# Optimization experiments

Hardware: AMD Instinct MI355X
Metric: run time of the kernel (lower is better)

Reference implementation:

```python
import jax, jax.numpy as jnp
import numpy as np

B, N, H, D, F_IN = 2, 2048, 8, 64, 512  # D = per-head dim (= out_features), H*D = model dim
EPS = 1e-5


def setup_inputs() -> dict:
    key = jax.random.key(0)
    k1, k2, k3 = jax.random.split(key, 3)
    x = jax.random.normal(k1, (B, N, F_IN), dtype=jnp.float32)
    adj = jax.random.randint(k2, (B, N, N), 0, 2, dtype=jnp.int32)
    W_w = jax.random.normal(k3, (F_IN, H * D), dtype=jnp.float32) / np.sqrt(F_IN).astype(np.float32)
    W_b = jnp.zeros((H * D,), dtype=jnp.float32)
    gamma = jnp.ones((H * D,), dtype=jnp.float32)
    beta = jnp.zeros((H * D,), dtype=jnp.float32)
    return {"x": x, "adj": adj, "W_w": W_w, "W_b": W_b, "gamma": gamma, "beta": beta}


def reference(x, adj, W_w, W_b, gamma, beta):
    b, n, _ = x.shape
    # shared projection: q = k = v
    h = (x @ W_w + W_b).reshape(b, n, H, D).transpose(0, 2, 1, 3)  # [B,H,N,D]
    attn = jnp.einsum("bhnd,bhmd->bhnm", h, h) * (D ** -0.5)       # [B,H,N,N]
    mask = (adj[:, None, :, :] != 0)                                 # broadcast over heads
    attn = jnp.where(mask, attn, -jnp.inf)
    attn = jax.nn.softmax(attn, axis=-1)
    out = jnp.einsum("bhnm,bhmd->bhnd", attn, h)                    # [B,H,N,D]
    out = out.transpose(0, 2, 1, 3).reshape(b, n, H * D)
    # LayerNorm over model dim
    mu = out.mean(axis=-1, keepdims=True)
    var = out.var(axis=-1, keepdims=True)
    out = (out - mu) * jax.lax.rsqrt(var + EPS) * gamma + beta
    return out, attn.mean(axis=1)
```

## Files before the change

### kernel.cpp

```cpp
#include <hip/hip_runtime.h>

typedef __attribute__((ext_vector_type(8))) short bf16x8;
typedef __attribute__((ext_vector_type(4))) short bf16x4;
typedef __attribute__((ext_vector_type(4))) float f32x4;
typedef __attribute__((ext_vector_type(2))) float f32x2;
typedef __attribute__((ext_vector_type(4))) _Float16 f16x4;
typedef __attribute__((ext_vector_type(2))) _Float16 f16x2;

static __device__ __forceinline__ f32x4 MFMA_QK(bf16x8 a, bf16x8 b, f32x4 c) {
  return __builtin_amdgcn_mfma_f32_16x16x32_bf16(a, b, c, 0, 0, 0);
}

#if __has_builtin(__builtin_amdgcn_mfma_f32_16x16x16bf16_1k)
static __device__ __forceinline__ f32x4 MFMA_PV(bf16x4 a, bf16x4 b, f32x4 c) {
  return __builtin_amdgcn_mfma_f32_16x16x16bf16_1k(a, b, c, 0, 0, 0);
}
#define PV_EPILOGUE_GUARD()
#else
static __device__ __forceinline__ f32x4 MFMA_PV(bf16x4 a, bf16x4 b, f32x4 c) {
  asm("v_mfma_f32_16x16x16_bf16 %0, %1, %2, %0" : "+v"(c) : "v"(a), "v"(b));
  return c;
}
#define PV_EPILOGUE_GUARD() asm volatile("s_nop 7\ns_nop 7" :::)
#endif

#if __has_builtin(__builtin_amdgcn_exp2f)
#define EXP2(x) __builtin_amdgcn_exp2f(x)
#else
#define EXP2(x) exp2f(x)
#endif

#define NB   2
#define NSEQ 2048
#define NH   8
#define ND   64
#define FIN  512
#define MD   512
#define NTOK (NB * NSEQ)
#define SCALE_LOG2E 0.18033688011112042f

#define XB_ELEMS   (NTOK * FIN)
#define WT_ELEMS   (MD * FIN)
#define HH_ELEMS   (NB * NH * NSEQ * ND)
#define MB_ELEMS   (NTOK * 32)
#define L_ELEMS    (NB * NH * NSEQ)
#define O_ELEMS    (NTOK * MD)
#define NSPLIT_S   8
#define NSPLIT_A   4

static __device__ __forceinline__ unsigned short f2b(float f) {
  union { float f; unsigned u; } c; c.f = f;
  unsigned u = c.u;
  u += 0x7fffu + ((u >> 16) & 1u);
  return (unsigned short)(u >> 16);
}

static __device__ __forceinline__ unsigned pack2(float a, float b) {
#if __has_builtin(__builtin_amdgcn_cvt_pk_bf16_f32)
  auto v = __builtin_amdgcn_cvt_pk_bf16_f32(a, b);
  unsigned r; __builtin_memcpy(&r, &v, 4); return r;
#else
  return (unsigned)f2b(a) | ((unsigned)f2b(b) << 16);
#endif
}

static __device__ __forceinline__ void split8(bf16x8 v, bf16x4* a, bf16x4* b) {
  union { bf16x8 w; bf16x4 h[2]; } u; u.w = v; *a = u.h[0]; *b = u.h[1];
}

__global__ __launch_bounds__(256)
void cvt_kernel(const float* __restrict__ x, const float* __restrict__ W,
                unsigned short* __restrict__ xb, unsigned short* __restrict__ wt) {
  const int t = threadIdx.x;
  if (blockIdx.x < 2048) {
    size_t i = ((size_t)blockIdx.x * 256 + t) * 4;
    f32x4 v = *(const f32x4*)(x + i);
    ushort4 o = make_ushort4(f2b(v[0]), f2b(v[1]), f2b(v[2]), f2b(v[3]));
    *(ushort4*)(xb + i) = o;
  } else {
    int j = ((int)(blockIdx.x - 2048) * 256 + t) * 4;
    int k = j >> 9, n = j & 511;
    f32x4 v = *(const f32x4*)(W + (size_t)k * MD + n);
    wt[(size_t)(n + 0) * FIN + k] = f2b(v[0]);
    wt[(size_t)(n + 1) * FIN + k] = f2b(v[1]);
    wt[(size_t)(n + 2) * FIN + k] = f2b(v[2]);
    wt[(size_t)(n + 3) * FIN + k] = f2b(v[3]);
  }
}

__global__ __launch_bounds__(1024)
void maskpack_kernel(const int* __restrict__ adj, unsigned long long* __restrict__ mb) {
  const int t = threadIdx.x;
  const int gw = blockIdx.x * 16 + (t >> 6);
  const int row = gw >> 5, w64 = gw & 31;
  int a = adj[(size_t)row * NSEQ + w64 * 64 + (t & 63)];
  unsigned long long m = __ballot(a != 0);
  if ((t & 63) == 0) mb[gw] = m;
}

__global__ __launch_bounds__(256, 2)
void proj_kernel(const unsigned short* __restrict__ xb, const unsigned short* __restrict__ wt,
                 const float* __restrict__ bias,
                 unsigned short* __restrict__ h_c, unsigned short* __restrict__ h_v) {
  __shared__ __align__(16) unsigned short sA[64][72];
  __shared__ __align__(16) unsigned short sB[64][72];
  const int t = threadIdx.x;
  const int w = t >> 6, L = t & 63, l15 = L & 15, qd = L >> 4;
  const int bm = blockIdx.x, bn = blockIdx.y;
  const int r = t >> 3, c8 = (t & 7) * 8;
  const f32x4 ZERO4 = {0.f, 0.f, 0.f, 0.f};

  f32x4 acc[4];
  #pragma unroll
  for (int q = 0; q < 4; ++q) acc[q] = ZERO4;

  for (int ks = 0; ks < FIN; ks += 64) {
    __syncthreads();
    *(bf16x8*)&sA[r][c8]      = *(const bf16x8*)&xb[(size_t)(bm*64 + r)      * FIN + ks + c8];
    *(bf16x8*)&sA[r + 32][c8] = *(const bf16x8*)&xb[(size_t)(bm*64 + r + 32) * FIN + ks + c8];
    *(bf16x8*)&sB[r][c8]      = *(const bf16x8*)&wt[(size_t)(bn*64 + r)      * FIN + ks + c8];
    *(bf16x8*)&sB[r + 32][c8] = *(const bf16x8*)&wt[(size_t)(bn*64 + r + 32) * FIN + ks + c8];
    __syncthreads();
    #pragma unroll
    for (int kk = 0; kk < 2; ++kk) {
      bf16x8 af = *(const bf16x8*)&sA[16*w + l15][kk*32 + qd*8];
      #pragma unroll
      for (int q = 0; q < 4; ++q) {
        bf16x8 bf = *(const bf16x8*)&sB[16*q + l15][kk*32 + qd*8];
        acc[q] = MFMA_QK(af, bf, acc[q]);
      }
    }
  }

  #pragma unroll
  for (int q = 0; q < 4; ++q) {
    int feat = bn * 64 + 16 * q + l15;
    int hh = feat >> 6, d = feat & 63;
    float bv = bias[feat];
    int token0 = bm * 64 + 16 * w + qd * 4;
    int b0 = token0 >> 11, nn0 = token0 & 2047;
    size_t hcb = (size_t)(b0 * NH + hh) * HH_ELEMS / (NB * NH);
    unsigned short pk[4];
    #pragma unroll
    for (int rr = 0; rr < 4; ++rr) {
      float v = acc[q][rr] + bv;
      unsigned short bb = f2b(v);
      int n = nn0 + rr;
      size_t idx = hcb + ((size_t)(n >> 4)) * 1024 + (d >> 5) * 512
                 + ((d >> 3) & 3) * 128 + (n & 15) * 8 + (d & 7);
      h_c[idx] = bb;
      pk[rr] = bb;
    }
    size_t vidx = hcb + ((size_t)(nn0 >> 4)) * 1024 + ((d >> 5)) * 512
                + (((nn0 >> 2) & 3) * 16 + (d & 15)) * 8 + ((d >> 4) & 1) * 4;
    *(ushort4*)&h_v[vidx] = make_ushort4(pk[0], pk[1], pk[2], pk[3]);
  }
}

__global__ __launch_bounds__(512, 4)
void stats_kernel(const unsigned short* __restrict__ h_c,
                  const unsigned long long* __restrict__ mb,
                  float* __restrict__ l_part) {
  const int t = threadIdx.x;
  const int h = t >> 6, L = t & 63, l15 = L & 15, qd = L >> 4;
  const int u = blockIdx.x & 7;
  const int b = u >> 2;
  const int rblk = ((int)blockIdx.x >> 3) * 4 + (u & 3);
  const int q8 = blockIdx.y;
  const int n0 = rblk * 32;
  const int qd4 = qd * 4;
  const int lane8 = L * 8;
  const f32x4 ZERO4 = {0.f, 0.f, 0.f, 0.f};

  const unsigned short* hc = h_c + (size_t)(b * NH + h) * (NSEQ * ND);
  bf16x8 qf[2][2];
  #pragma unroll
  for (int g = 0; g < 2; ++g)
    #pragma unroll
    for (int kk = 0; kk < 2; ++kk)
      qf[g][kk] = *(const bf16x8*)&hc[((n0 >> 4) + g) * 1024 + kk * 512 + lane8];

  float lacc[2] = {0.f, 0.f};
  const unsigned long long* mrow = mb + (((size_t)(b * NSEQ + n0 + l15)) << 5) + q8 * 4;

  for (int it = 0; it < 4; ++it) {
    const int c0 = q8 * 256 + it * 64;
    unsigned mlo[2], mhi[2];
    #pragma unroll
    for (int g = 0; g < 2; ++g) {
      unsigned long long m = mrow[g * 512 + it];
      mlo[g] = (unsigned)m; mhi[g] = (unsigned)(m >> 32);
    }
    #pragma unroll
    for (int cc = 0; cc < 4; ++cc) {
      const int cb = (c0 >> 4) + cc;
      bf16x8 kf0 = *(const bf16x8*)&hc[cb * 1024 + lane8];
      bf16x8 kf1 = *(const bf16x8*)&hc[cb * 1024 + 512 + lane8];
      #pragma unroll
      for (int g = 0; g < 2; ++g) {
        f32x4 s = MFMA_QK(kf0, qf[g][0], ZERO4);
        s = MFMA_QK(kf1, qf[g][1], s);
        unsigned nib = (((cc & 2) ? mhi[g] : mlo[g]) >> (((cc & 1) << 4) + qd4)) & 0xFu;
        #pragma unroll
        for (int rr = 0; rr < 4; ++rr) {
          float e = EXP2(s[rr] * SCALE_LOG2E);
          lacc[g] += (nib & (1u << rr)) ? e : 0.f;
        }
      }
    }
  }
  #pragma unroll
  for (int g = 0; g < 2; ++g) {
    float v = lacc[g];
    v += __shfl_xor(v, 16);
    v += __shfl_xor(v, 32);
    if (L < 16)
      l_part[(size_t)q8 * L_ELEMS + (size_t)(b * NH + h) * NSEQ + n0 + g*16 + L] = v;
  }
}

__global__ __launch_bounds__(512, 4)
void attn_kernel(const unsigned short* __restrict__ h_c, const unsigned short* __restrict__ h_v,
                 const unsigned long long* __restrict__ mb, const float* __restrict__ l_part,
                 _Float16* __restrict__ o_part, float* __restrict__ mean_out) {
  const int t = threadIdx.x;
  const int h = t >> 6, L = t & 63, l15 = L & 15, qd = L >> 4;
  const int u = blockIdx.x & 7;
  const int b = u >> 2;
  const int rblk = ((int)blockIdx.x >> 3) * 4 + (u & 3);
  const int quarter = blockIdx.y;
  const int n0 = rblk * 32;
  const int qd4 = qd * 4;
  const int lane8 = L * 8;
  __shared__ __align__(16) unsigned short s_part[2][8][32][72];
  const f32x4 ZERO4 = {0.f, 0.f, 0.f, 0.f};

  const unsigned short* hc = h_c + (size_t)(b * NH + h) * (NSEQ * ND);
  const unsigned short* hv = h_v + (size_t)(b * NH + h) * (NSEQ * ND);

  bf16x8 qf[2][2];
  #pragma unroll
  for (int g = 0; g < 2; ++g)
    #pragma unroll
    for (int kk = 0; kk < 2; ++kk)
      qf[g][kk] = *(const bf16x8*)&hc[((n0 >> 4) + g) * 1024 + kk * 512 + lane8];

  float linv[2];
  #pragma unroll
  for (int g = 0; g < 2; ++g) {
    size_t idx = (size_t)(b * NH + h) * NSEQ + n0 + g*16 + l15;
    float ls = 0.f;
    #pragma unroll
    for (int q = 0; q < NSPLIT_S; ++q) ls += l_part[(size_t)q * L_ELEMS + idx];
    linv[g] = -__log2f(ls);
  }

  f32x4 oacc[2][4];
  #pragma unroll
  for (int g = 0; g < 2; ++g)
    #pragma unroll
    for (int dc = 0; dc < 4; ++dc) oacc[g][dc] = ZERO4;

  const int cr = t >> 4, cc4 = (t & 15) * 4;
  const unsigned long long* mrow = mb + (((size_t)(b * NSEQ + n0 + l15)) << 5) + quarter * 8;

  for (int it = 0; it < 8; ++it) {
    const int c0 = quarter * 512 + it * 64;
    const int buf = it & 1;
    unsigned mlo[2], mhi[2];
    #pragma unroll
    for (int g = 0; g < 2; ++g) {
      unsigned long long m = mrow[g * 512 + it];
      mlo[g] = (unsigned)m; mhi[g] = (unsigned)(m >> 32);
    }
    #pragma unroll
    for (int cc = 0; cc < 4; ++cc) {
      const int cb = (c0 >> 4) + cc;
      bf16x8 kf0 = *(const bf16x8*)&hc[cb * 1024 + lane8];
      bf16x8 kf1 = *(const bf16x8*)&hc[cb * 1024 + 512 + lane8];
      bf16x8 vv0 = *(const bf16x8*)&hv[cb * 1024 + lane8];
      bf16x8 vv1 = *(const bf16x8*)&hv[cb * 1024 + 512 + lane8];
      bf16x4 va[4];
      split8(vv0, &va[0], &va[1]);
      split8(vv1, &va[2], &va[3]);
      #pragma unroll
      for (int g = 0; g < 2; ++g) {
        f32x4 s = MFMA_QK(kf0, qf[g][0], ZERO4);
        s = MFMA_QK(kf1, qf[g][1], s);
        unsigned nib = (((cc & 2) ? mhi[g] : mlo[g]) >> (((cc & 1) << 4) + qd4)) & 0xFu;
        f32x4 p;
        #pragma unroll
        for (int rr = 0; rr < 4; ++rr) {
          float e = EXP2(__builtin_fmaf(s[rr], SCALE_LOG2E, linv[g]));
          p[rr] = (nib & (1u << rr)) ? e : 0.f;
        }
        union { unsigned u2[2]; bf16x4 v4; uint2 d; } pk;
        pk.u2[0] = pack2(p[0], p[1]);
        pk.u2[1] = pack2(p[2], p[3]);
        *(uint2*)&s_part[buf][h][g*16 + l15][cc*16 + qd4] = pk.d;
        #pragma unroll
        for (int dc = 0; dc < 4; ++dc)
          oacc[g][dc] = MFMA_PV(va[dc], pk.v4, oacc[g][dc]);
      }
    }
    __syncthreads();
    {
      f32x4 macc = ZERO4;
      #pragma unroll
      for (int hh = 0; hh < 8; ++hh) {
        uint2 pv = *(const uint2*)&s_part[buf][hh][cr][cc4];
        union { unsigned u; float f; } a0, a1, a2, a3;
        a0.u = pv.x << 16; a1.u = pv.x & 0xffff0000u;
        a2.u = pv.y << 16; a3.u = pv.y & 0xffff0000u;
        macc[0] += a0.f; macc[1] += a1.f; macc[2] += a2.f; macc[3] += a3.f;
      }
      macc *= 0.125f;
      *(f32x4*)&mean_out[((size_t)b * NSEQ + n0 + cr) * NSEQ + c0 + cc4] = macc;
    }
  }

  PV_EPILOGUE_GUARD();
  #pragma unroll
  for (int g = 0; g < 2; ++g)
    #pragma unroll
    for (int dc = 0; dc < 4; ++dc) {
      size_t token = (size_t)b * NSEQ + n0 + g*16 + l15;
      f16x4 o;
      #pragma unroll
      for (int rr = 0; rr < 4; ++rr) o[rr] = (_Float16)oacc[g][dc][rr];
      *(f16x4*)&o_part[(size_t)quarter * O_ELEMS + token * MD + h*64 + dc*16 + qd4] = o;
    }
}

__global__ __launch_bounds__(256)
void ln_kernel(const _Float16* __restrict__ o_part, const float* __restrict__ gamma,
               const float* __restrict__ beta, float* __restrict__ out) {
  const int row = blockIdx.x, t = threadIdx.x;
  const size_t base = (size_t)row * MD + 2 * t;
  float v0 = 0.f, v1 = 0.f;
  #pragma unroll
  for (int q = 0; q < NSPLIT_A; ++q) {
    f16x2 x = *(const f16x2*)&o_part[(size_t)q * O_ELEMS + base];
    v0 += (float)x[0]; v1 += (float)x[1];
  }
  float s = v0 + v1, sq = v0 * v0 + v1 * v1;
  for (int m = 1; m < 64; m <<= 1) { s += __shfl_xor(s, m); sq += __shfl_xor(sq, m); }
  __shared__ float rs[4], rq[4];
  if ((t & 63) == 0) { rs[t >> 6] = s; rq[t >> 6] = sq; }
  __syncthreads();
  s = rs[0] + rs[1] + rs[2] + rs[3];
  sq = rq[0] + rq[1] + rq[2] + rq[3];
  float mu = s * (1.f / MD);
  float var = sq * (1.f / MD) - mu * mu;
  float rstd = rsqrtf(var + 1e-5f);
  f32x2 g2 = *(const f32x2*)&gamma[2 * t];
  f32x2 b2 = *(const f32x2*)&beta[2 * t];
  f32x2 o;
  o[0] = (v0 - mu) * rstd * g2[0] + b2[0];
  o[1] = (v1 - mu) * rstd * g2[1] + b2[1];
  *(f32x2*)&out[base] = o;
}

extern "C" void kernel_launch(void* const* d_in, const int* in_sizes, int n_in,
                              void* d_out, int out_size, void* d_ws, size_t ws_size,
                              hipStream_t stream) {
  const float* x     = (const float*)d_in[0];
  const int*   adj   = (const int*)d_in[1];
  const float* W     = (const float*)d_in[2];
  const float* Wb    = (const float*)d_in[3];
  const float* gamma = (const float*)d_in[4];
  const float* beta  = (const float*)d_in[5];
  float* out = (float*)d_out;

  unsigned short* xb  = (unsigned short*)d_ws;
  unsigned short* wt  = xb + XB_ELEMS;
  unsigned short* h_c = wt + WT_ELEMS;
  unsigned short* h_v = h_c + HH_ELEMS;
  unsigned long long* mbits = (unsigned long long*)(h_v + HH_ELEMS);
  float* l_part = (float*)(mbits + MB_ELEMS);
  _Float16* o_part = (_Float16*)(l_part + NSPLIT_S * L_ELEMS);

  cvt_kernel<<<2304, 256, 0, stream>>>(x, W, xb, wt);
  maskpack_kernel<<<8192, 1024, 0, stream>>>(adj, mbits);
  proj_kernel<<<dim3(64, 8), 256, 0, stream>>>(xb, wt, Wb, h_c, h_v);
  stats_kernel<<<dim3(128, NSPLIT_S), 512, 0, stream>>>(h_c, mbits, l_part);
  attn_kernel<<<dim3(128, NSPLIT_A), 512, 0, stream>>>(h_c, h_v, mbits, l_part, o_part,
                                                       out + (size_t)NTOK * MD);
  ln_kernel<<<NTOK, 256, 0, stream>>>(o_part, gamma, beta, out);
}
```

Baseline: 186.0 us.

## Split attention across eighths with atomic fp32 output and transposed projection stores

The attention kernel's key-column split goes from four to eight, so twice as many blocks launch. Partial outputs are now summed with fp32 atomicAdd into one zeroed buffer, replacing per-quarter fp16 partials that layer norm had to add up. The LDS double buffer for the per-head probabilities becomes a single buffer with an extra barrier. The projection kernel computes a second, transposed MFMA accumulator so h_c can be written with vectorized ushort4 stores instead of scalar scattered stores. The costs are doubled projection MFMA work, a memset, and atomic contention on the output.

```diff
diff --git a/kernel.cpp b/kernel.cpp
--- a/kernel.cpp
+++ b/kernel.cpp
@@ -4,8 +4,6 @@
 typedef __attribute__((ext_vector_type(4))) short bf16x4;
 typedef __attribute__((ext_vector_type(4))) float f32x4;
 typedef __attribute__((ext_vector_type(2))) float f32x2;
-typedef __attribute__((ext_vector_type(4))) _Float16 f16x4;
-typedef __attribute__((ext_vector_type(2))) _Float16 f16x2;
 
 static __device__ __forceinline__ f32x4 MFMA_QK(bf16x8 a, bf16x8 b, f32x4 c) {
   return __builtin_amdgcn_mfma_f32_16x16x32_bf16(a, b, c, 0, 0, 0);
@@ -46,7 +44,7 @@
 #define L_ELEMS    (NB * NH * NSEQ)
 #define O_ELEMS    (NTOK * MD)
 #define NSPLIT_S   8
-#define NSPLIT_A   4
+#define NSPLIT_A   8
 
 static __device__ __forceinline__ unsigned short f2b(float f) {
   union { float f; unsigned u; } c; c.f = f;
@@ -110,9 +108,9 @@
   const int r = t >> 3, c8 = (t & 7) * 8;
   const f32x4 ZERO4 = {0.f, 0.f, 0.f, 0.f};
 
-  f32x4 acc[4];
-  #pragma unroll
-  for (int q = 0; q < 4; ++q) acc[q] = ZERO4;
+  f32x4 acc_v[4], acc_c[4];
+  #pragma unroll
+  for (int q = 0; q < 4; ++q) { acc_v[q] = ZERO4; acc_c[q] = ZERO4; }
 
   for (int ks = 0; ks < FIN; ks += 64) {
     __syncthreads();
@@ -127,33 +125,40 @@
       #pragma unroll
       for (int q = 0; q < 4; ++q) {
         bf16x8 bf = *(const bf16x8*)&sB[16*q + l15][kk*32 + qd*8];
-        acc[q] = MFMA_QK(af, bf, acc[q]);
+        acc_v[q] = MFMA_QK(af, bf, acc_v[q]);
+        acc_c[q] = MFMA_QK(bf, af, acc_c[q]);
       }
     }
   }
 
+  const int head = bn;
+  const int b0 = bm >> 5;
+  const int nloc = (bm & 31) * 64;
+  const size_t slab = (size_t)(b0 * NH + head) * ((size_t)NSEQ * ND);
+
   #pragma unroll
   for (int q = 0; q < 4; ++q) {
-    int feat = bn * 64 + 16 * q + l15;
-    int hh = feat >> 6, d = feat & 63;
-    float bv = bias[feat];
-    int token0 = bm * 64 + 16 * w + qd * 4;
-    int b0 = token0 >> 11, nn0 = token0 & 2047;
-    size_t hcb = (size_t)(b0 * NH + hh) * HH_ELEMS / (NB * NH);
+    int d = 16*q + l15;
+    float bv = bias[bn*64 + d];
     unsigned short pk[4];
     #pragma unroll
-    for (int rr = 0; rr < 4; ++rr) {
-      float v = acc[q][rr] + bv;
-      unsigned short bb = f2b(v);
-      int n = nn0 + rr;
-      size_t idx = hcb + ((size_t)(n >> 4)) * 1024 + (d >> 5) * 512
-                 + ((d >> 3) & 3) * 128 + (n & 15) * 8 + (d & 7);
-      h_c[idx] = bb;
-      pk[rr] = bb;
-    }
-    size_t vidx = hcb + ((size_t)(nn0 >> 4)) * 1024 + ((d >> 5)) * 512
-                + (((nn0 >> 2) & 3) * 16 + (d & 15)) * 8 + ((d >> 4) & 1) * 4;
+    for (int rr = 0; rr < 4; ++rr) pk[rr] = f2b(acc_v[q][rr] + bv);
+    int n0 = nloc + 16*w + qd*4;
+    size_t vidx = slab + (size_t)(n0 >> 4) * 1024 + (size_t)(d >> 5) * 512
+                + (size_t)((((n0 >> 2) & 3) * 16 + (d & 15)) * 8) + (size_t)(((d >> 4) & 1) * 4);
     *(ushort4*)&h_v[vidx] = make_ushort4(pk[0], pk[1], pk[2], pk[3]);
+  }
+  #pragma unroll
+  for (int q = 0; q < 4; ++q) {
+    int dbase = 16*q + 4*qd;
+    f32x4 bv4 = *(const f32x4*)&bias[bn*64 + dbase];
+    unsigned short pk[4];
+    #pragma unroll
+    for (int rr = 0; rr < 4; ++rr) pk[rr] = f2b(acc_c[q][rr] + bv4[rr]);
+    int n = nloc + 16*w + l15;
+    size_t cidx = slab + (size_t)(n >> 4) * 1024 + (size_t)(q >> 1) * 512
+                + (size_t)(((dbase >> 3) & 3) * 128) + (size_t)((n & 15) * 8) + (size_t)(dbase & 7);
+    *(ushort4*)&h_c[cidx] = make_ushort4(pk[0], pk[1], pk[2], pk[3]);
   }
 }
 
@@ -222,17 +227,17 @@
 __global__ __launch_bounds__(512, 4)
 void attn_kernel(const unsigned short* __restrict__ h_c, const unsigned short* __restrict__ h_v,
                  const unsigned long long* __restrict__ mb, const float* __restrict__ l_part,
-                 _Float16* __restrict__ o_part, float* __restrict__ mean_out) {
+                 float* __restrict__ o_acc, float* __restrict__ mean_out) {
   const int t = threadIdx.x;
   const int h = t >> 6, L = t & 63, l15 = L & 15, qd = L >> 4;
   const int u = blockIdx.x & 7;
   const int b = u >> 2;
   const int rblk = ((int)blockIdx.x >> 3) * 4 + (u & 3);
-  const int quarter = blockIdx.y;
+  const int eighth = blockIdx.y;
   const int n0 = rblk * 32;
   const int qd4 = qd * 4;
   const int lane8 = L * 8;
-  __shared__ __align__(16) unsigned short s_part[2][8][32][72];
+  __shared__ __align__(16) unsigned short s_part[8][32][72];
   const f32x4 ZERO4 = {0.f, 0.f, 0.f, 0.f};
 
   const unsigned short* hc = h_c + (size_t)(b * NH + h) * (NSEQ * ND);
@@ -262,17 +267,17 @@
     for (int dc = 0; dc < 4; ++dc) oacc[g][dc] = ZERO4;
 
   const int cr = t >> 4, cc4 = (t & 15) * 4;
-  const unsigned long long* mrow = mb + (((size_t)(b * NSEQ + n0 + l15)) << 5) + quarter * 8;
-
-  for (int it = 0; it < 8; ++it) {
-    const int c0 = quarter * 512 + it * 64;
-    const int buf = it & 1;
+  const unsigned long long* mrow = mb + (((size_t)(b * NSEQ + n0 + l15)) << 5) + eighth * 4;
+
+  for (int it = 0; it < 4; ++it) {
+    const int c0 = eighth * 256 + it * 64;
     unsigned mlo[2], mhi[2];
     #pragma unroll
     for (int g = 0; g < 2; ++g) {
       unsigned long long m = mrow[g * 512 + it];
       mlo[g] = (unsigned)m; mhi[g] = (unsigned)(m >> 32);
     }
+    __syncthreads();
     #pragma unroll
     for (int cc = 0; cc < 4; ++cc) {
       const int cb = (c0 >> 4) + cc;
@@ -297,7 +302,7 @@
         union { unsigned u2[2]; bf16x4 v4; uint2 d; } pk;
         pk.u2[0] = pack2(p[0], p[1]);
         pk.u2[1] = pack2(p[2], p[3]);
-        *(uint2*)&s_part[buf][h][g*16 + l15][cc*16 + qd4] = pk.d;
+        *(uint2*)&s_part[h][g*16 + l15][cc*16 + qd4] = pk.d;
         #pragma unroll
         for (int dc = 0; dc < 4; ++dc)
           oacc[g][dc] = MFMA_PV(va[dc], pk.v4, oacc[g][dc]);
@@ -308,7 +313,7 @@
       f32x4 macc = ZERO4;
       #pragma unroll
       for (int hh = 0; hh < 8; ++hh) {
-        uint2 pv = *(const uint2*)&s_part[buf][hh][cr][cc4];
+        uint2 pv = *(const uint2*)&s_part[hh][cr][cc4];
         union { unsigned u; float f; } a0, a1, a2, a3;
         a0.u = pv.x << 16; a1.u = pv.x & 0xffff0000u;
         a2.u = pv.y << 16; a3.u = pv.y & 0xffff0000u;
@@ -325,24 +330,19 @@
     #pragma unroll
     for (int dc = 0; dc < 4; ++dc) {
       size_t token = (size_t)b * NSEQ + n0 + g*16 + l15;
-      f16x4 o;
-      #pragma unroll
-      for (int rr = 0; rr < 4; ++rr) o[rr] = (_Float16)oacc[g][dc][rr];
-      *(f16x4*)&o_part[(size_t)quarter * O_ELEMS + token * MD + h*64 + dc*16 + qd4] = o;
+      float* dst = &o_acc[token * MD + h*64 + dc*16 + qd4];
+      #pragma unroll
+      for (int rr = 0; rr < 4; ++rr) atomicAdd(dst + rr, oacc[g][dc][rr]);
     }
 }
 
 __global__ __launch_bounds__(256)
-void ln_kernel(const _Float16* __restrict__ o_part, const float* __restrict__ gamma,
+void ln_kernel(const float* __restrict__ o_acc, const float* __restrict__ gamma,
                const float* __restrict__ beta, float* __restrict__ out) {
   const int row = blockIdx.x, t = threadIdx.x;
   const size_t base = (size_t)row * MD + 2 * t;
-  float v0 = 0.f, v1 = 0.f;
-  #pragma unroll
-  for (int q = 0; q < NSPLIT_A; ++q) {
-    f16x2 x = *(const f16x2*)&o_part[(size_t)q * O_ELEMS + base];
-    v0 += (float)x[0]; v1 += (float)x[1];
-  }
+  f32x2 x = *(const f32x2*)&o_acc[base];
+  float v0 = x[0], v1 = x[1];
   float s = v0 + v1, sq = v0 * v0 + v1 * v1;
   for (int m = 1; m < 64; m <<= 1) { s += __shfl_xor(s, m); sq += __shfl_xor(sq, m); }
   __shared__ float rs[4], rq[4];
@@ -378,13 +378,14 @@
   unsigned short* h_v = h_c + HH_ELEMS;
   unsigned long long* mbits = (unsigned long long*)(h_v + HH_ELEMS);
   float* l_part = (float*)(mbits + MB_ELEMS);
-  _Float16* o_part = (_Float16*)(l_part + NSPLIT_S * L_ELEMS);
-
+  float* o_acc = l_part + NSPLIT_S * L_ELEMS;
+
+  hipMemsetAsync(o_acc, 0, (size_t)O_ELEMS * sizeof(float), stream);
   cvt_kernel<<<2304, 256, 0, stream>>>(x, W, xb, wt);
   maskpack_kernel<<<8192, 1024, 0, stream>>>(adj, mbits);
   proj_kernel<<<dim3(64, 8), 256, 0, stream>>>(xb, wt, Wb, h_c, h_v);
   stats_kernel<<<dim3(128, NSPLIT_S), 512, 0, stream>>>(h_c, mbits, l_part);
-  attn_kernel<<<dim3(128, NSPLIT_A), 512, 0, stream>>>(h_c, h_v, mbits, l_part, o_part,
+  attn_kernel<<<dim3(128, NSPLIT_A), 512, 0, stream>>>(h_c, h_v, mbits, l_part, o_acc,
                                                        out + (size_t)NTOK * MD);
-  ln_kernel<<<NTOK, 256, 0, stream>>>(o_part, gamma, beta, out);
-}
+  ln_kernel<<<NTOK, 256, 0, stream>>>(o_acc, gamma, beta, out);
+}
```

Measured after the change: 374.3 us. 101% more time.
